# Optimization experiments

Hardware: AMD Instinct MI355X
Metric: run time of the kernel (lower is better)

Reference implementation:

```python
import math
import jax, jax.numpy as jnp
import numpy as np

N_TOKENS = 32768
N_TYPES = 21
D_MODEL = 1024
N_SEQS = 64


def setup_inputs() -> dict:
    key = jax.random.key(0)
    k1, k2, k3, k4 = jax.random.split(key, 4)
    x = jax.random.normal(k1, (N_TOKENS, N_TYPES), dtype=jnp.float32)
    # nn.Linear(n_types, d_model): weight [d_model, n_types], bias [d_model]
    W = jax.random.normal(k2, (D_MODEL, N_TYPES), dtype=jnp.float32) / math.sqrt(N_TYPES)
    b = jax.random.normal(k3, (D_MODEL,), dtype=jnp.float32) * 0.01
    # sorted segment ids -> ragged batch of N_SEQS sequences
    batch = jnp.sort(jax.random.randint(k4, (N_TOKENS,), 0, N_SEQS, dtype=jnp.int64))
    return {"x": x, "W": W, "b": b, "batch": batch}


def _position_encoding(max_len, d_model, dtype):
    pos = jnp.arange(max_len, dtype=jnp.float32)[:, None]          # [L,1]
    div = jnp.exp(jnp.arange(0, d_model, 2, dtype=jnp.float32) * (-math.log(10000.0) / d_model))
    ang = pos * div                                                 # [L, d/2]
    pe = jnp.zeros((max_len, d_model), dtype=jnp.float32)
    pe = pe.at[:, 0::2].set(jnp.sin(ang)).at[:, 1::2].set(jnp.cos(ang))
    return pe.astype(dtype)


def reference(x, W, b, batch):
    d_model = W.shape[0]
    # Linear projection + sqrt(d_model) scale
    h = (jnp.einsum('nt,dt->nd', x, W) + b) * math.sqrt(d_model)    # [N, d_model]

    # pad_batch: relabel via unique ids, compute per-token position within its
    # sequence, and scatter into a padded [n_seqs, max_len, d_model] tensor.
    bnp = np.asarray(batch)
    _, inv, counts = np.unique(bnp, return_inverse=True, return_counts=True)
    n_seqs = counts.shape[0]
    max_len = int(counts.max())
    offsets = np.concatenate([np.zeros(1, dtype=np.int64), np.cumsum(counts)[:-1]])
    pos = np.arange(bnp.shape[0], dtype=np.int64) - offsets[inv]    # position within sequence

    padded = jnp.zeros((n_seqs, max_len, d_model), dtype=h.dtype)
    padded = padded.at[jnp.asarray(inv), jnp.asarray(pos)].set(h)

    # mask: True where valid token (original returns ~pad_mask)
    mask = jnp.arange(max_len)[None, :] < jnp.asarray(counts)[:, None]

    pe = _position_encoding(max_len, d_model, h.dtype)              # [L, d_model]
    out = padded + pe[None, :, :]
    return (out, mask)
```

## Files before the change

### kernel.cpp

```cpp
#include <hip/hip_runtime.h>
#include <hip/hip_bf16.h>
#include <math.h>

#define RPB 13
#define XSTR 24

typedef float f4 __attribute__((ext_vector_type(4)));

__global__ __launch_bounds__(1024) void setup_kernel(const int* __restrict__ batch,
                                                     int n, int* __restrict__ tables) {
  __shared__ int samp[256];
  __shared__ int csum[64];
  __shared__ int fine[64];
  __shared__ int sbase[64];
  __shared__ int lbs[65];
  __shared__ int stride_s;
  int t = threadIdx.x;
  if (t == 0) stride_s = (batch[n - 1] == 0) ? 2 : 1;
  if (t < 64) { csum[t] = 0; fine[t] = 0; }
  __syncthreads();
  int stride = stride_s;
  int window = (n + 255) >> 8;
  if (t < 256) {
    long long idx = (long long)t * window;
    if (idx > n - 1) idx = n - 1;
    samp[t] = batch[idx * stride];
  }
  __syncthreads();
  {
    int v = t >> 4, q = t & 15;
    int c = 0;
#pragma unroll
    for (int i = 0; i < 16; ++i) c += (samp[q * 16 + i] < v) ? 1 : 0;
    atomicAdd(&csum[v], c);
  }
  __syncthreads();
  if (t < 64) {
    int c = csum[t];
    sbase[t] = (c == 0) ? 0 : (c - 1) * window;
  }
  __syncthreads();
  {
    int v = t >> 4, q = t & 15;
    int wpt = (window + 15) >> 4;
    int S = sbase[v];
    int c = 0;
    for (int j = q * wpt; j < (q + 1) * wpt && j < window; ++j) {
      int idx = S + j;
      if (idx < n && batch[idx * stride] < v) c++;
    }
    atomicAdd(&fine[v], c);
  }
  __syncthreads();
  if (t < 64) {
    lbs[t] = sbase[t] + fine[t];
    if (t == 0) lbs[64] = n;
  }
  __syncthreads();
  if (t < 64) {
    int cnt = lbs[t + 1] - lbs[t];
    unsigned long long present = __ballot(cnt > 0);
    int seg = __popcll(present & ((1ull << t) - 1ull));
    int nseq = __popcll(present);
    if (cnt > 0) { tables[seg] = lbs[t]; tables[64 + seg] = cnt; }
    if (t >= nseq) { tables[t] = 0; tables[64 + t] = 0; }
  }
}

__global__ __launch_bounds__(256) void embed_kernel(
    const float* __restrict__ x, const float* __restrict__ W,
    const float* __restrict__ b, const int* __restrict__ tables,
    float* __restrict__ out, float* __restrict__ mask,
    int L, int totalRows, int n_tokens) {
  int t = threadIdx.x;
  __shared__ __align__(16) float xs[RPB * XSTR];

  int base = blockIdx.x * RPB;
  int s = base / L;
  int p0 = base - s * L;
  int st = tables[s];
  int cnt = tables[64 + s];
  int pc = p0 < cnt ? p0 : cnt;
  int t0 = st + pc;

  {
    int gbase = t0 * 21;
    int glast = n_tokens * 21 - 1;
#pragma unroll
    for (int it = 0; it < (RPB * 21 + 255) / 256; ++it) {
      int u = t + it * 256;
      if (u < RPB * 21) {
        int li = u / 21;
        int j = u - li * 21;
        int g = gbase + u;
        if (g > glast) g = glast;
        xs[li * XSTR + j] = x[g];
      }
    }
  }

  if (t < RPB) {
    int row = base + t;
    if (row < totalRows) {
      int ss = row / L;
      int pp = row - ss * L;
      mask[row] = (pp < tables[64 + ss]) ? 1.0f : 0.0f;
    }
  }

  float wf[84];
  {
    const f4* wp = (const f4*)(W + 84 * t);
#pragma unroll
    for (int k = 0; k < 21; ++k) {
      f4 v = wp[k];
      wf[4 * k] = v[0]; wf[4 * k + 1] = v[1]; wf[4 * k + 2] = v[2]; wf[4 * k + 3] = v[3];
    }
  }
  f4 bb = *(const f4*)(b + 4 * t);

  const float KC = -0.01798894603901599f;
  float divA = __expf(KC * (float)(2 * t));
  float divB = __expf(KC * (float)(2 * t + 1));
  float dsA, dcA, dsB, dcB, sA, cA, sB, cB;
  __sincosf(divA, &dsA, &dcA);
  __sincosf(divB, &dsB, &dcB);
  __sincosf((float)p0 * divA, &sA, &cA);
  __sincosf((float)p0 * divB, &sB, &cB);

  __syncthreads();

  int p = p0;
  int li = 0;
  int nrows = totalRows - base; if (nrows > RPB) nrows = RPB;
  float* po = out + (size_t)base * 1024 + 4 * t;

  for (int rr = 0; rr < nrows; ++rr) {
    bool valid = (p < cnt);
    f4 res; res[0] = sA; res[1] = cA; res[2] = sB; res[3] = cB;
    if (valid) {
      const f4* xr = (const f4*)&xs[li * XSTR];
      f4 v0 = xr[0], v1 = xr[1], v2 = xr[2], v3 = xr[3], v4 = xr[4];
      float xk[21];
#pragma unroll
      for (int q = 0; q < 4; ++q) {
        xk[q] = v0[q]; xk[4 + q] = v1[q]; xk[8 + q] = v2[q]; xk[12 + q] = v3[q];
        xk[16 + q] = v4[q];
      }
      xk[20] = xs[li * XSTR + 20];
      float a0 = bb[0], a1 = bb[1], a2 = bb[2], a3 = bb[3];
#pragma unroll
      for (int k = 0; k < 21; ++k) {
        float xv = xk[k];
        a0 = fmaf(xv, wf[k], a0);
        a1 = fmaf(xv, wf[21 + k], a1);
        a2 = fmaf(xv, wf[42 + k], a2);
        a3 = fmaf(xv, wf[63 + k], a3);
      }
      res[0] = fmaf(a0, 32.f, res[0]);
      res[1] = fmaf(a1, 32.f, res[1]);
      res[2] = fmaf(a2, 32.f, res[2]);
      res[3] = fmaf(a3, 32.f, res[3]);
      ++li;
    }
    *(f4*)po = res;
    po += 1024;

    if (rr + 1 < nrows) {
      ++p;
      if (p == L) {
        p = 0; ++s;
        st = tables[s]; cnt = tables[64 + s];
        sA = 0.f; cA = 1.f; sB = 0.f; cB = 1.f;
      } else {
        float nsA = fmaf(sA, dcA, cA * dsA);
        float ncA = fmaf(cA, dcA, -sA * dsA);
        float nsB = fmaf(sB, dcB, cB * dsB);
        float ncB = fmaf(cB, dcB, -sB * dsB);
        sA = nsA; cA = ncA; sB = nsB; cB = ncB;
      }
    }
  }
}

extern "C" void kernel_launch(void* const* d_in, const int* in_sizes, int n_in,
                              void* d_out, int out_size, void* d_ws, size_t ws_size,
                              hipStream_t stream) {
  const float* x = (const float*)d_in[0];
  const float* W = (const float*)d_in[1];
  const float* b = (const float*)d_in[2];
  const int* batch = (const int*)d_in[3];
  int n_tokens = in_sizes[3];
  float* out = (float*)d_out;

  int L = out_size / (64 * 1025);
  int totalRows = 64 * L;

  int* tables = (int*)d_ws;

  setup_kernel<<<1, 1024, 0, stream>>>(batch, n_tokens, tables);
  int grid = (totalRows + RPB - 1) / RPB;
  embed_kernel<<<grid, 256, 0, stream>>>(x, W, b, tables, out,
                                         out + (size_t)totalRows * 1024,
                                         L, totalRows, n_tokens);
}
```

Baseline: 47.40 us.

## Double rows per block, add single-segment fast path with direct sincos

Raises rows per block from 13 to 26 and sets a launch-bounds minimum of 2 blocks per CU. Adds a fast path for blocks whose rows all lie in one sequence: it computes the positional encoding per row with sincos instead of the serial rotation recurrence, which removes the loop-carried dependency and allows unrolling. Blocks that cross a sequence boundary use a slow path that also computes sincos directly. The change trades extra transcendental work per row for more independent work and fewer blocks, and the new launch bound may cap registers for the 84-float weight array and cause spills.

```diff
diff --git a/kernel.cpp b/kernel.cpp
--- a/kernel.cpp
+++ b/kernel.cpp
@@ -2,7 +2,7 @@
 #include <hip/hip_bf16.h>
 #include <math.h>
 
-#define RPB 13
+#define RPB 26
 #define XSTR 24
 
 typedef float f4 __attribute__((ext_vector_type(4)));
@@ -67,7 +67,7 @@
   }
 }
 
-__global__ __launch_bounds__(256) void embed_kernel(
+__global__ __launch_bounds__(256, 2) void embed_kernel(
     const float* __restrict__ x, const float* __restrict__ W,
     const float* __restrict__ b, const int* __restrict__ tables,
     float* __restrict__ out, float* __restrict__ mask,
@@ -122,24 +122,23 @@
   const float KC = -0.01798894603901599f;
   float divA = __expf(KC * (float)(2 * t));
   float divB = __expf(KC * (float)(2 * t + 1));
-  float dsA, dcA, dsB, dcB, sA, cA, sB, cB;
-  __sincosf(divA, &dsA, &dcA);
-  __sincosf(divB, &dsB, &dcB);
-  __sincosf((float)p0 * divA, &sA, &cA);
-  __sincosf((float)p0 * divB, &sB, &cB);
-
-  __syncthreads();
-
-  int p = p0;
-  int li = 0;
-  int nrows = totalRows - base; if (nrows > RPB) nrows = RPB;
+
+  __syncthreads();
+
   float* po = out + (size_t)base * 1024 + 4 * t;
-
-  for (int rr = 0; rr < nrows; ++rr) {
-    bool valid = (p < cnt);
-    f4 res; res[0] = sA; res[1] = cA; res[2] = sB; res[3] = cB;
-    if (valid) {
-      const f4* xr = (const f4*)&xs[li * XSTR];
+  bool fast = (base + RPB <= totalRows) && ((base + RPB - 1) / L == s);
+
+  if (fast) {
+    int nvalid = cnt - p0;
+    if (nvalid < 0) nvalid = 0;
+#pragma unroll 2
+    for (int rr = 0; rr < RPB; ++rr) {
+      bool valid = rr < nvalid;
+      float fp = (float)(p0 + rr);
+      float s0, c0, s1, c1;
+      __sincosf(fp * divA, &s0, &c0);
+      __sincosf(fp * divB, &s1, &c1);
+      const f4* xr = (const f4*)&xs[rr * XSTR];
       f4 v0 = xr[0], v1 = xr[1], v2 = xr[2], v3 = xr[3], v4 = xr[4];
       float xk[21];
 #pragma unroll
@@ -147,7 +146,7 @@
         xk[q] = v0[q]; xk[4 + q] = v1[q]; xk[8 + q] = v2[q]; xk[12 + q] = v3[q];
         xk[16 + q] = v4[q];
       }
-      xk[20] = xs[li * XSTR + 20];
+      xk[20] = xs[rr * XSTR + 20];
       float a0 = bb[0], a1 = bb[1], a2 = bb[2], a3 = bb[3];
 #pragma unroll
       for (int k = 0; k < 21; ++k) {
@@ -157,27 +156,52 @@
         a2 = fmaf(xv, wf[42 + k], a2);
         a3 = fmaf(xv, wf[63 + k], a3);
       }
-      res[0] = fmaf(a0, 32.f, res[0]);
-      res[1] = fmaf(a1, 32.f, res[1]);
-      res[2] = fmaf(a2, 32.f, res[2]);
-      res[3] = fmaf(a3, 32.f, res[3]);
-      ++li;
-    }
-    *(f4*)po = res;
-    po += 1024;
-
-    if (rr + 1 < nrows) {
-      ++p;
-      if (p == L) {
-        p = 0; ++s;
-        st = tables[s]; cnt = tables[64 + s];
-        sA = 0.f; cA = 1.f; sB = 0.f; cB = 1.f;
-      } else {
-        float nsA = fmaf(sA, dcA, cA * dsA);
-        float ncA = fmaf(cA, dcA, -sA * dsA);
-        float nsB = fmaf(sB, dcB, cB * dsB);
-        float ncB = fmaf(cB, dcB, -sB * dsB);
-        sA = nsA; cA = ncA; sB = nsB; cB = ncB;
+      f4 res;
+      res[0] = valid ? fmaf(a0, 32.f, s0) : s0;
+      res[1] = valid ? fmaf(a1, 32.f, c0) : c0;
+      res[2] = valid ? fmaf(a2, 32.f, s1) : s1;
+      res[3] = valid ? fmaf(a3, 32.f, c1) : c1;
+      *(f4*)(po + (size_t)rr * 1024) = res;
+    }
+  } else {
+    int p = p0, li = 0;
+    int nrows = totalRows - base; if (nrows > RPB) nrows = RPB;
+    for (int rr = 0; rr < nrows; ++rr) {
+      bool valid = (p < cnt);
+      float fp = (float)p;
+      float s0, c0, s1, c1;
+      __sincosf(fp * divA, &s0, &c0);
+      __sincosf(fp * divB, &s1, &c1);
+      f4 res; res[0] = s0; res[1] = c0; res[2] = s1; res[3] = c1;
+      if (valid) {
+        const f4* xr = (const f4*)&xs[li * XSTR];
+        f4 v0 = xr[0], v1 = xr[1], v2 = xr[2], v3 = xr[3], v4 = xr[4];
+        float xk[21];
+#pragma unroll
+        for (int q = 0; q < 4; ++q) {
+          xk[q] = v0[q]; xk[4 + q] = v1[q]; xk[8 + q] = v2[q]; xk[12 + q] = v3[q];
+          xk[16 + q] = v4[q];
+        }
+        xk[20] = xs[li * XSTR + 20];
+        float a0 = bb[0], a1 = bb[1], a2 = bb[2], a3 = bb[3];
+#pragma unroll
+        for (int k = 0; k < 21; ++k) {
+          float xv = xk[k];
+          a0 = fmaf(xv, wf[k], a0);
+          a1 = fmaf(xv, wf[21 + k], a1);
+          a2 = fmaf(xv, wf[42 + k], a2);
+          a3 = fmaf(xv, wf[63 + k], a3);
+        }
+        res[0] = fmaf(a0, 32.f, res[0]);
+        res[1] = fmaf(a1, 32.f, res[1]);
+        res[2] = fmaf(a2, 32.f, res[2]);
+        res[3] = fmaf(a3, 32.f, res[3]);
+        ++li;
+      }
+      *(f4*)(po + (size_t)rr * 1024) = res;
+      if (rr + 1 < nrows) {
+        ++p;
+        if (p == L) { p = 0; ++s; st = tables[s]; cnt = tables[64 + s]; }
       }
     }
   }
```

After: 45.63 us. -3.7%, faster.
